# Kernel optimization log

Hardware: AMD Instinct MI355X
Metric: run time of the kernel (lower is better)

## Reference

```python
import jax, jax.numpy as jnp
import numpy as np
from math import sqrt

# dims
B, H, P, N, D = 4, 8, 32, 32, 16   # batch, heads, n_patches, channels, patch_len
L = P * N                           # 1024 token positions
SEQ, PRED, WIN, E, NF = 512, 96, 10, 2, 6  # seq_len, pred_len, attention_window, e_layers, n_fore
EPS = float(np.finfo(np.float32).eps)      # torch RMSNorm default eps (finfo eps)


def setup_inputs() -> dict:
    key = jax.random.key(0)
    ks = jax.random.split(key, 8)
    return dict(
        tokens=jax.random.normal(ks[0], (B, H, L, D), jnp.float32),
        x_original=jax.random.normal(ks[1], (B, SEQ, N), jnp.float32),
        log_scales=jnp.full((E,), np.log(2.0), jnp.float32),
        attn_norm_w=jnp.ones((E, D), jnp.float32),
        conv_up_w=jax.random.normal(ks[2], (E, 2 * H, 1, 3), jnp.float32) * 0.1,
        conv_down_w=jax.random.normal(ks[3], (E, H, 2, 1), jnp.float32) * 0.1,
        ffn_norm_w=jnp.ones((E, D), jnp.float32),
        mix_w=jax.random.normal(ks[4], (1, H), jnp.float32) * 0.3,
        mix_b=jnp.zeros((1,), jnp.float32),
        fore_w=jax.random.normal(ks[5], (NF, P), jnp.float32) * 0.1,
        fore_b=jnp.zeros((NF,), jnp.float32),
    )


def _rms(x, w):
    # torch.nn.RMSNorm over last dim (patch_len)
    return x * jax.lax.rsqrt(jnp.mean(x * x, axis=-1, keepdims=True) + EPS) * w


def _mask():
    # pid repeated per-channel; True entries are masked out
    pid = jnp.repeat(jnp.arange(P), N)
    diff = pid[None, :] - pid[:, None]  # pid[key] - pid[query]
    return (diff <= 0) | (diff >= WIN)  # [L, L]


def _signed_attn(h, log_scale, mask):
    # scores: [B,H,L,L]; A = softmax(+s) - softmax(-s) with banded mask
    scores = jnp.einsum('bhld,bhmd->bhlm', h, h)
    scale = jnp.clip(jnp.exp(log_scale), 1.0, 30.0) / sqrt(D)
    pos = jnp.where(mask, -10000.0, scores)
    neg = jnp.where(mask, -10000.0, -scores)
    A = jax.nn.softmax(scale * pos, axis=-1) - jax.nn.softmax(scale * neg, axis=-1)
    return jnp.einsum('bhlm,bhmd->bhld', A, h)


def _conv_ffn(x, up_w, down_w, norm_w):
    # depthwise causal conv along patch time dim D; x: [B,H,L,D]
    r = x.transpose(0, 2, 1, 3).reshape(B * L, H, D)
    r = jnp.pad(r, ((0, 0), (0, 0), (2, 0)))  # causal left-pad (kernel_size-1)
    dn = ('NCH', 'OIH', 'NCH')
    r = jax.lax.conv_general_dilated(r, up_w, (1,), 'VALID', dimension_numbers=dn, feature_group_count=H)
    r = jax.nn.gelu(r, approximate=False)
    r = jax.lax.conv_general_dilated(r, down_w, (1,), 'VALID', dimension_numbers=dn, feature_group_count=H)
    r = r.reshape(B, L, H, D).transpose(0, 2, 1, 3)
    return _rms(x + r, norm_w)


def reference(tokens, x_original, log_scales, attn_norm_w, conv_up_w, conv_down_w,
              ffn_norm_w, mix_w, mix_b, fore_w, fore_b):
    mask = _mask()
    h = tokens
    for l in range(E):
        h = _rms(h + _signed_attn(h, log_scales[l], mask), attn_norm_w[l])
        h = _conv_ffn(h, conv_up_w[l], conv_down_w[l], ffn_norm_w[l])
    # aggregate heads -> forecast
    h = h.reshape(B, H, P, N, D).transpose(0, 3, 4, 2, 1)       # (B,N,D,P,H)
    h = jnp.einsum('bndph,h->bndp', h, mix_w[0]) + mix_b[0]      # channel_mixing
    f = jnp.einsum('bndp,fp->bndf', h, fore_w) + fore_b          # fore_projection
    f = f.reshape(B, N, D * NF)[:, :, -PRED:]                    # flatten + tail slice
    forecast = f.transpose(0, 2, 1)                              # (B,pred_len,N)
    return forecast, x_original
```

## Files before the change

### kernel.cpp

```cpp
#include <hip/hip_runtime.h>
#include <hip/hip_bf16.h>
#include <math.h>

#define BB 4
#define HH 8
#define PP 32
#define NN 32
#define DD 16
#define LL 1024
#define WINW 10
#define NFF 6
#define PREDL 96
#define SEQL 512
#define EPSF 1.1920928955078125e-07f
#define KROW 24
#define KTS 296
#define PROW 40
#define XROW 20

typedef __attribute__((ext_vector_type(8))) short bf16x8;
typedef __attribute__((ext_vector_type(4))) float f32x4;

__device__ inline short f2bs(float f) {
    __hip_bfloat16 h = __float2bfloat16(f);
    return *reinterpret_cast<short*>(&h);
}

__global__ __launch_bounds__(128) void layer_kernel(
    const float* __restrict__ hin, float* __restrict__ hout,
    const float* __restrict__ log_scales, const float* __restrict__ attn_norm,
    const float* __restrict__ up_w, const float* __restrict__ down_w,
    const float* __restrict__ ffn_norm, int layer)
{
    __shared__ short hK[9 * 32 * KROW];
    __shared__ short VT[16 * KTS];
    __shared__ short Pp[2][16 * PROW];
    __shared__ short Pn[2][16 * PROW];
    __shared__ float xls[32 * XROW];

    int blk = blockIdx.x;
    int bh  = blk >> 5;
    int hh  = bh & 7;
    int p0  = blk & 31;
    int nstage = min(9, (PP - 1) - p0);

    int tid  = threadIdx.x;
    int wid  = tid >> 6;
    int lane = tid & 63;
    int quad = lane >> 4, n16 = lane & 15;

    {
        const float4* src = (const float4*)(hin + ((size_t)bh * LL + (p0 + 1) * NN) * DD);
        if (nstage == 9) {
            #pragma unroll
            for (int k = 0; k < 9; ++k) {
                int i = tid + k * 128;
                int row = i >> 2, j = i & 3;
                float4 v = src[i];
                short s0 = f2bs(v.x), s1 = f2bs(v.y), s2 = f2bs(v.z), s3 = f2bs(v.w);
                unsigned long long u =
                      (unsigned long long)(unsigned short)s0
                    | ((unsigned long long)(unsigned short)s1 << 16)
                    | ((unsigned long long)(unsigned short)s2 << 32)
                    | ((unsigned long long)(unsigned short)s3 << 48);
                *(unsigned long long*)&hK[row * KROW + j * 4] = u;
                int d0 = j * 4;
                VT[(d0 + 0) * KTS + row] = s0;
                VT[(d0 + 1) * KTS + row] = s1;
                VT[(d0 + 2) * KTS + row] = s2;
                VT[(d0 + 3) * KTS + row] = s3;
            }
        } else {
            int nf4 = nstage * 128;
            for (int i = tid; i < nf4; i += 128) {
                int row = i >> 2, j = i & 3;
                float4 v = src[i];
                short s0 = f2bs(v.x), s1 = f2bs(v.y), s2 = f2bs(v.z), s3 = f2bs(v.w);
                unsigned long long u =
                      (unsigned long long)(unsigned short)s0
                    | ((unsigned long long)(unsigned short)s1 << 16)
                    | ((unsigned long long)(unsigned short)s2 << 32)
                    | ((unsigned long long)(unsigned short)s3 << 48);
                *(unsigned long long*)&hK[row * KROW + j * 4] = u;
                int d0 = j * 4;
                VT[(d0 + 0) * KTS + row] = s0;
                VT[(d0 + 1) * KTS + row] = s1;
                VT[(d0 + 2) * KTS + row] = s2;
                VT[(d0 + 3) * KTS + row] = s3;
            }
        }
    }

    bf16x8 Aq;
    #pragma unroll
    for (int j = 0; j < 8; ++j) Aq[j] = 0;
    if (quad < 2) {
        const float* qp = hin + ((size_t)bh * LL + p0 * NN + wid * 16 + n16) * DD + quad * 8;
        #pragma unroll
        for (int j = 0; j < 8; ++j) Aq[j] = f2bs(qp[j]);
    }
    float rs[4];
    #pragma unroll
    for (int r = 0; r < 4; ++r)
        rs[r] = hin[((size_t)bh * LL + p0 * NN + wid * 16 + quad * 4 + r) * DD + n16];

    float sc = fminf(fmaxf(__expf(log_scales[layer]), 1.0f), 30.0f) * 0.25f;

    __syncthreads();

    f32x4 Op, On;
    Op[0] = Op[1] = Op[2] = Op[3] = 0.f;
    On[0] = On[1] = On[2] = On[3] = 0.f;
    float lpp[4] = {0.f, 0.f, 0.f, 0.f}, lnn[4] = {0.f, 0.f, 0.f, 0.f};
    short* myPp = Pp[wid];
    short* myPn = Pn[wid];

    for (int c = 0; c < nstage; ++c) {
        int kb = c * 32;
        #pragma unroll
        for (int kt = 0; kt < 2; ++kt) {
            bf16x8 Bk;
            #pragma unroll
            for (int j = 0; j < 8; ++j) Bk[j] = 0;
            if (quad < 2)
                Bk = *(const bf16x8*)&hK[(kb + kt * 16 + n16) * KROW + quad * 8];
            f32x4 z; z[0] = z[1] = z[2] = z[3] = 0.f;
            f32x4 S = __builtin_amdgcn_mfma_f32_16x16x32_bf16(Aq, Bk, z, 0, 0, 0);
            #pragma unroll
            for (int r = 0; r < 4; ++r) {
                float s  = S[r];
                float ep = __expf(sc * s);
                float en = __expf(-sc * s);
                lpp[r] += ep; lnn[r] += en;
                int pr = quad * 4 + r, pc = kt * 16 + n16;
                myPp[pr * PROW + pc] = f2bs(ep);
                myPn[pr * PROW + pc] = f2bs(en);
            }
        }
        bf16x8 Bv = *(const bf16x8*)&VT[n16 * KTS + kb + quad * 8];
        bf16x8 Ap = *(const bf16x8*)&myPp[n16 * PROW + quad * 8];
        bf16x8 An = *(const bf16x8*)&myPn[n16 * PROW + quad * 8];
        Op = __builtin_amdgcn_mfma_f32_16x16x32_bf16(Ap, Bv, Op, 0, 0, 0);
        On = __builtin_amdgcn_mfma_f32_16x16x32_bf16(An, Bv, On, 0, 0, 0);
    }

    #pragma unroll
    for (int r = 0; r < 4; ++r) {
        float a = lpp[r], b = lnn[r];
        a += __shfl_xor(a, 1); a += __shfl_xor(a, 2); a += __shfl_xor(a, 4); a += __shfl_xor(a, 8);
        b += __shfl_xor(b, 1); b += __shfl_xor(b, 2); b += __shfl_xor(b, 4); b += __shfl_xor(b, 8);
        lpp[r] = a; lnn[r] = b;
    }

    #pragma unroll
    for (int r = 0; r < 4; ++r) {
        float lp = lpp[r], ln = lnn[r];
        float rl = (lp > 0.f) ? (1.0f / lp) : 0.f;
        float rn = (ln > 0.f) ? (1.0f / ln) : 0.f;
        float v  = rs[r] + Op[r] * rl - On[r] * rn;
        float ss = v * v;
        ss += __shfl_xor(ss, 1); ss += __shfl_xor(ss, 2);
        ss += __shfl_xor(ss, 4); ss += __shfl_xor(ss, 8);
        float rr = rsqrtf(ss * (1.0f / 16.0f) + EPSF);
        xls[(wid * 16 + quad * 4 + r) * XROW + n16] = v * rr * attn_norm[layer * DD + n16];
    }

    if (lane < 16) {
        int q = wid * 16 + lane;
        float x[16];
        #pragma unroll
        for (int j = 0; j < 4; ++j) {
            float4 v = *(const float4*)&xls[q * XROW + j * 4];
            x[j*4+0] = v.x; x[j*4+1] = v.y; x[j*4+2] = v.z; x[j*4+3] = v.w;
        }

        const float* uw = up_w + (size_t)(layer * 2 * HH + 2 * hh) * 3;
        float w00 = uw[0], w01 = uw[1], w02 = uw[2];
        float w10 = uw[3], w11 = uw[4], w12 = uw[5];
        const float* dw = down_w + (size_t)(layer * HH + hh) * 2;
        float dc0 = dw[0], dc1 = dw[1];

        float v[16], ss = 0.f;
        #pragma unroll
        for (int i = 0; i < 16; ++i) {
            float xm2 = (i >= 2) ? x[i - 2] : 0.f;
            float xm1 = (i >= 1) ? x[i - 1] : 0.f;
            float u0 = w00 * xm2 + w01 * xm1 + w02 * x[i];
            float u1 = w10 * xm2 + w11 * xm1 + w12 * x[i];
            float g0 = 0.5f * u0 * (1.0f + erff(u0 * 0.7071067811865475f));
            float g1 = 0.5f * u1 * (1.0f + erff(u1 * 0.7071067811865475f));
            float vv = x[i] + dc0 * g0 + dc1 * g1;
            v[i] = vv; ss += vv * vv;
        }
        float r2 = rsqrtf(ss * (1.0f / 16.0f) + EPSF);
        float* op = hout + ((size_t)bh * LL + p0 * NN + q) * DD;
        #pragma unroll
        for (int i = 0; i < 16; ++i) op[i] = v[i] * r2 * ffn_norm[layer * DD + i];
    }
}

__global__ void tail_kernel(const float* __restrict__ h, const float* __restrict__ mw_,
                            const float* __restrict__ mb_, const float* __restrict__ fw_,
                            const float* __restrict__ fb_, const float* __restrict__ x,
                            float* __restrict__ out)
{
    int t = blockIdx.x * 256 + threadIdx.x;
    if (t < BB * DD * NFF * NN) {
        int n = t & 31;
        int r = t >> 5;
        int fi = r % NFF; r /= NFF;
        int d = r & 15;
        int b = r >> 4;

        float mw[8];
        #pragma unroll
        for (int k = 0; k < 8; ++k) mw[k] = mw_[k];
        float mb = mb_[0];

        float acc = fb_[fi];
        for (int p = 0; p < PP; ++p) {
            float m = mb;
            #pragma unroll
            for (int k = 0; k < 8; ++k)
                m += h[(size_t)(((b * HH + k) * LL) + p * NN + n) * DD + d] * mw[k];
            acc += m * fw_[fi * PP + p];
        }
        out[t] = acc;
    } else {
        int u4 = t - BB * DD * NFF * NN;
        if (u4 < BB * SEQL * NN / 4) {
            const float4* x4 = (const float4*)x;
            float4* o4 = (float4*)(out + BB * PREDL * NN);
            o4[u4] = x4[u4];
        }
    }
}

static int find_by_size(const int* s, int n, int want, int occurrence) {
    int seen = 0;
    for (int i = 0; i < n; ++i)
        if (s[i] == want) { if (seen == occurrence) return i; ++seen; }
    return -1;
}

extern "C" void kernel_launch(void* const* d_in, const int* in_sizes, int n_in,
                              void* d_out, int out_size, void* d_ws, size_t ws_size,
                              hipStream_t stream) {
    int it  = find_by_size(in_sizes, n_in, 524288, 0);
    int ix  = find_by_size(in_sizes, n_in, 65536, 0);
    int ils = find_by_size(in_sizes, n_in, 2, 0);
    int ian = find_by_size(in_sizes, n_in, 32, 0);
    int icu = find_by_size(in_sizes, n_in, 96, 0);
    int icd = find_by_size(in_sizes, n_in, 32, 1);
    int ifn = find_by_size(in_sizes, n_in, 32, 2);
    int imw = find_by_size(in_sizes, n_in, 8, 0);
    int imb = find_by_size(in_sizes, n_in, 1, 0);
    int ifw = find_by_size(in_sizes, n_in, 192, 0);
    int ifb = find_by_size(in_sizes, n_in, 6, 0);
    if (it < 0 || ix < 0 || ils < 0 || ian < 0 || icu < 0 || icd < 0 ||
        ifn < 0 || imw < 0 || imb < 0 || ifw < 0 || ifb < 0) {
        it = 0; ix = 1; ils = 2; ian = 3; icu = 4; icd = 5; ifn = 6;
        imw = 7; imb = 8; ifw = 9; ifb = 10;
    }

    const float* tokens     = (const float*)d_in[it];
    const float* x_orig     = (const float*)d_in[ix];
    const float* log_scales = (const float*)d_in[ils];
    const float* attn_norm  = (const float*)d_in[ian];
    const float* up_w       = (const float*)d_in[icu];
    const float* down_w     = (const float*)d_in[icd];
    const float* ffn_norm   = (const float*)d_in[ifn];
    const float* mix_w      = (const float*)d_in[imw];
    const float* mix_b      = (const float*)d_in[imb];
    const float* fore_w     = (const float*)d_in[ifw];
    const float* fore_b     = (const float*)d_in[ifb];
    float* out = (float*)d_out;

    const size_t NH = (size_t)BB * HH * LL * DD;
    float* hA = (float*)d_ws;
    float* hB = hA + NH;

    layer_kernel<<<1024, 128, 0, stream>>>(tokens, hA, log_scales, attn_norm,
                                           up_w, down_w, ffn_norm, 0);
    layer_kernel<<<1024, 128, 0, stream>>>(hA, hB, log_scales, attn_norm,
                                           up_w, down_w, ffn_norm, 1);
    const int tail_threads = BB * DD * NFF * NN + BB * SEQL * NN / 4;
    tail_kernel<<<(tail_threads + 255) / 256, 256, 0, stream>>>(
        hB, mix_w, mix_b, fore_w, fore_b, x_orig, out);
}
```

Baseline: 132.7 us.

## Split key stages across two waves per query tile and parallelize conv-FFN epilogue

Doubles the block to 256 threads so each 16-query tile is handled by two waves that each process half the key stages; partial outputs and softmax sums are merged through shared memory. The conv-FFN epilogue now uses all 64 lanes, with each lane computing four of the 16 positions, a cross-lane RMS reduction and float4 stores, in place of 16 serial lanes. exp is replaced by exp2 with a prescaled factor. The goal is to cut the serial latency per block, at the cost of an extra barrier, more shared memory and an uneven split (4 vs up to 5 stages).

After: 134.3 us. Within noise of the previous version (+1.2%).

```diff
diff --git a/kernel.cpp b/kernel.cpp
--- a/kernel.cpp
+++ b/kernel.cpp
@@ -26,7 +26,7 @@
     return *reinterpret_cast<short*>(&h);
 }
 
-__global__ __launch_bounds__(128) void layer_kernel(
+__global__ __launch_bounds__(256) void layer_kernel(
     const float* __restrict__ hin, float* __restrict__ hout,
     const float* __restrict__ log_scales, const float* __restrict__ attn_norm,
     const float* __restrict__ up_w, const float* __restrict__ down_w,
@@ -34,9 +34,11 @@
 {
     __shared__ short hK[9 * 32 * KROW];
     __shared__ short VT[16 * KTS];
-    __shared__ short Pp[2][16 * PROW];
-    __shared__ short Pn[2][16 * PROW];
+    __shared__ short Pp[4][16 * PROW];
+    __shared__ short Pn[4][16 * PROW];
     __shared__ float xls[32 * XROW];
+    __shared__ float comb[2][64][8];
+    __shared__ float combl[2][2][16];
 
     int blk = blockIdx.x;
     int bh  = blk >> 5;
@@ -46,15 +48,18 @@
 
     int tid  = threadIdx.x;
     int wid  = tid >> 6;
+    int qh   = wid >> 1;
+    int ch   = wid & 1;
     int lane = tid & 63;
     int quad = lane >> 4, n16 = lane & 15;
 
     {
         const float4* src = (const float4*)(hin + ((size_t)bh * LL + (p0 + 1) * NN) * DD);
-        if (nstage == 9) {
-            #pragma unroll
-            for (int k = 0; k < 9; ++k) {
-                int i = tid + k * 128;
+        int nf4 = nstage * 128;
+        #pragma unroll
+        for (int k = 0; k < 5; ++k) {
+            int i = tid + k * 256;
+            if (i < nf4) {
                 int row = i >> 2, j = i & 3;
                 float4 v = src[i];
                 short s0 = f2bs(v.x), s1 = f2bs(v.y), s2 = f2bs(v.z), s3 = f2bs(v.w);
@@ -70,24 +75,6 @@
                 VT[(d0 + 2) * KTS + row] = s2;
                 VT[(d0 + 3) * KTS + row] = s3;
             }
-        } else {
-            int nf4 = nstage * 128;
-            for (int i = tid; i < nf4; i += 128) {
-                int row = i >> 2, j = i & 3;
-                float4 v = src[i];
-                short s0 = f2bs(v.x), s1 = f2bs(v.y), s2 = f2bs(v.z), s3 = f2bs(v.w);
-                unsigned long long u =
-                      (unsigned long long)(unsigned short)s0
-                    | ((unsigned long long)(unsigned short)s1 << 16)
-                    | ((unsigned long long)(unsigned short)s2 << 32)
-                    | ((unsigned long long)(unsigned short)s3 << 48);
-                *(unsigned long long*)&hK[row * KROW + j * 4] = u;
-                int d0 = j * 4;
-                VT[(d0 + 0) * KTS + row] = s0;
-                VT[(d0 + 1) * KTS + row] = s1;
-                VT[(d0 + 2) * KTS + row] = s2;
-                VT[(d0 + 3) * KTS + row] = s3;
-            }
         }
     }
 
@@ -95,16 +82,19 @@
     #pragma unroll
     for (int j = 0; j < 8; ++j) Aq[j] = 0;
     if (quad < 2) {
-        const float* qp = hin + ((size_t)bh * LL + p0 * NN + wid * 16 + n16) * DD + quad * 8;
+        const float* qp = hin + ((size_t)bh * LL + p0 * NN + qh * 16 + n16) * DD + quad * 8;
         #pragma unroll
         for (int j = 0; j < 8; ++j) Aq[j] = f2bs(qp[j]);
     }
-    float rs[4];
-    #pragma unroll
-    for (int r = 0; r < 4; ++r)
-        rs[r] = hin[((size_t)bh * LL + p0 * NN + wid * 16 + quad * 4 + r) * DD + n16];
-
-    float sc = fminf(fmaxf(__expf(log_scales[layer]), 1.0f), 30.0f) * 0.25f;
+    float rs[4] = {0.f, 0.f, 0.f, 0.f};
+    if (ch == 0) {
+        #pragma unroll
+        for (int r = 0; r < 4; ++r)
+            rs[r] = hin[((size_t)bh * LL + p0 * NN + qh * 16 + quad * 4 + r) * DD + n16];
+    }
+
+    float sc  = fminf(fmaxf(__expf(log_scales[layer]), 1.0f), 30.0f) * 0.25f;
+    float sc2 = sc * 1.4426950408889634f;
 
     __syncthreads();
 
@@ -115,7 +105,10 @@
     short* myPp = Pp[wid];
     short* myPn = Pn[wid];
 
-    for (int c = 0; c < nstage; ++c) {
+    int c0 = ch ? 4 : 0;
+    int c1 = ch ? nstage : min(4, nstage);
+
+    for (int c = c0; c < c1; ++c) {
         int kb = c * 32;
         #pragma unroll
         for (int kt = 0; kt < 2; ++kt) {
@@ -128,9 +121,9 @@
             f32x4 S = __builtin_amdgcn_mfma_f32_16x16x32_bf16(Aq, Bk, z, 0, 0, 0);
             #pragma unroll
             for (int r = 0; r < 4; ++r) {
-                float s  = S[r];
-                float ep = __expf(sc * s);
-                float en = __expf(-sc * s);
+                float t  = sc2 * S[r];
+                float ep = exp2f(t);
+                float en = exp2f(-t);
                 lpp[r] += ep; lnn[r] += en;
                 int pr = quad * 4 + r, pc = kt * 16 + n16;
                 myPp[pr * PROW + pc] = f2bs(ep);
@@ -150,6 +143,32 @@
         a += __shfl_xor(a, 1); a += __shfl_xor(a, 2); a += __shfl_xor(a, 4); a += __shfl_xor(a, 8);
         b += __shfl_xor(b, 1); b += __shfl_xor(b, 2); b += __shfl_xor(b, 4); b += __shfl_xor(b, 8);
         lpp[r] = a; lnn[r] = b;
+    }
+
+    if (ch == 1) {
+        *(f32x4*)&comb[qh][lane][0] = Op;
+        *(f32x4*)&comb[qh][lane][4] = On;
+        if (n16 == 0) {
+            #pragma unroll
+            for (int r = 0; r < 4; ++r) {
+                combl[qh][0][quad * 4 + r] = lpp[r];
+                combl[qh][1][quad * 4 + r] = lnn[r];
+            }
+        }
+    }
+    __syncthreads();
+    if (ch == 1) return;
+
+    {
+        f32x4 o2 = *(const f32x4*)&comb[qh][lane][0];
+        f32x4 n2 = *(const f32x4*)&comb[qh][lane][4];
+        #pragma unroll
+        for (int r = 0; r < 4; ++r) {
+            Op[r] += o2[r];
+            On[r] += n2[r];
+            lpp[r] += combl[qh][0][quad * 4 + r];
+            lnn[r] += combl[qh][1][quad * 4 + r];
+        }
     }
 
     #pragma unroll
@@ -162,17 +181,12 @@
         ss += __shfl_xor(ss, 1); ss += __shfl_xor(ss, 2);
         ss += __shfl_xor(ss, 4); ss += __shfl_xor(ss, 8);
         float rr = rsqrtf(ss * (1.0f / 16.0f) + EPSF);
-        xls[(wid * 16 + quad * 4 + r) * XROW + n16] = v * rr * attn_norm[layer * DD + n16];
-    }
-
-    if (lane < 16) {
-        int q = wid * 16 + lane;
-        float x[16];
-        #pragma unroll
-        for (int j = 0; j < 4; ++j) {
-            float4 v = *(const float4*)&xls[q * XROW + j * 4];
-            x[j*4+0] = v.x; x[j*4+1] = v.y; x[j*4+2] = v.z; x[j*4+3] = v.w;
-        }
+        xls[(qh * 16 + quad * 4 + r) * XROW + n16] = v * rr * attn_norm[layer * DD + n16];
+    }
+
+    {
+        int q = qh * 16 + n16;
+        int g = quad;
 
         const float* uw = up_w + (size_t)(layer * 2 * HH + 2 * hh) * 3;
         float w00 = uw[0], w01 = uw[1], w02 = uw[2];
@@ -180,22 +194,32 @@
         const float* dw = down_w + (size_t)(layer * HH + hh) * 2;
         float dc0 = dw[0], dc1 = dw[1];
 
-        float v[16], ss = 0.f;
-        #pragma unroll
-        for (int i = 0; i < 16; ++i) {
-            float xm2 = (i >= 2) ? x[i - 2] : 0.f;
-            float xm1 = (i >= 1) ? x[i - 1] : 0.f;
-            float u0 = w00 * xm2 + w01 * xm1 + w02 * x[i];
-            float u1 = w10 * xm2 + w11 * xm1 + w12 * x[i];
+        float xm2 = g ? xls[q * XROW + 4 * g - 2] : 0.f;
+        float xm1 = g ? xls[q * XROW + 4 * g - 1] : 0.f;
+        float4 xv = *(const float4*)&xls[q * XROW + 4 * g];
+        float xa[6] = {xm2, xm1, xv.x, xv.y, xv.z, xv.w};
+
+        float v4[4], ss = 0.f;
+        #pragma unroll
+        for (int i = 0; i < 4; ++i) {
+            float u0 = w00 * xa[i] + w01 * xa[i + 1] + w02 * xa[i + 2];
+            float u1 = w10 * xa[i] + w11 * xa[i + 1] + w12 * xa[i + 2];
             float g0 = 0.5f * u0 * (1.0f + erff(u0 * 0.7071067811865475f));
             float g1 = 0.5f * u1 * (1.0f + erff(u1 * 0.7071067811865475f));
-            float vv = x[i] + dc0 * g0 + dc1 * g1;
-            v[i] = vv; ss += vv * vv;
-        }
+            float vv = xa[i + 2] + dc0 * g0 + dc1 * g1;
+            v4[i] = vv; ss += vv * vv;
+        }
+        ss += __shfl_xor(ss, 16); ss += __shfl_xor(ss, 32);
         float r2 = rsqrtf(ss * (1.0f / 16.0f) + EPSF);
-        float* op = hout + ((size_t)bh * LL + p0 * NN + q) * DD;
-        #pragma unroll
-        for (int i = 0; i < 16; ++i) op[i] = v[i] * r2 * ffn_norm[layer * DD + i];
+
+        const float4 fn = *(const float4*)&ffn_norm[layer * DD + 4 * g];
+        float* op = hout + ((size_t)bh * LL + p0 * NN + q) * DD + 4 * g;
+        float4 o;
+        o.x = v4[0] * r2 * fn.x;
+        o.y = v4[1] * r2 * fn.y;
+        o.z = v4[2] * r2 * fn.z;
+        o.w = v4[3] * r2 * fn.w;
+        *(float4*)op = o;
     }
 }
 
@@ -280,9 +304,9 @@
     float* hA = (float*)d_ws;
     float* hB = hA + NH;
 
-    layer_kernel<<<1024, 128, 0, stream>>>(tokens, hA, log_scales, attn_norm,
+    layer_kernel<<<1024, 256, 0, stream>>>(tokens, hA, log_scales, attn_norm,
                                            up_w, down_w, ffn_norm, 0);
-    layer_kernel<<<1024, 128, 0, stream>>>(hA, hB, log_scales, attn_norm,
+    layer_kernel<<<1024, 256, 0, stream>>>(hA, hB, log_scales, attn_norm,
                                            up_w, down_w, ffn_norm, 1);
     const int tail_threads = BB * DD * NFF * NN + BB * SEQL * NN / 4;
     tail_kernel<<<(tail_threads + 255) / 256, 256, 0, stream>>>(
```
